# Optimization experiments

Measured on AMD Instinct MI355X. Metric: run time of the kernel, lower is better.

The kernel has to match this reference:

```python
import jax, jax.numpy as jnp
import numpy as np

B, S, D = 256, 512, 768
SEP_ID = 2
BOS_ID = 0
PAD_ID = 1


def setup_inputs() -> dict:
    key = jax.random.key(0)
    k_h, = jax.random.split(key, 1)
    hidden_states = jax.random.normal(k_h, (B, S, D), dtype=jnp.float32)

    rng = np.random.default_rng(0)
    ids = rng.integers(5, 64000, size=(B, S), dtype=np.int64)
    mask = np.zeros((B, S), dtype=np.int64)
    title_len = rng.integers(3, 60, size=B)
    lead_len = rng.integers(10, 300, size=B)
    for i in range(B):
        tl, ll = int(title_len[i]), int(lead_len[i])
        ids[i, 0] = BOS_ID
        ids[i, 1 + tl] = SEP_ID          # first </s>
        ids[i, 2 + tl] = SEP_ID          # second </s>
        lead_end = 3 + tl + ll           # position of third </s>
        lead_end = min(lead_end, S - 1)
        ids[i, 3 + tl:lead_end] = rng.integers(5, 64000, size=lead_end - (3 + tl))
        ids[i, lead_end] = SEP_ID        # third </s>
        ids[i, lead_end + 1:] = PAD_ID
        mask[i, :lead_end + 1] = 1
    return {
        "hidden_states": hidden_states,
        "input_ids": jnp.asarray(ids),
        "attention_mask": jnp.asarray(mask),
        "sep_token_id": SEP_ID,
    }


def reference(hidden_states, input_ids, attention_mask, sep_token_id):
    Bsz, Slen, _ = hidden_states.shape
    idx = jnp.arange(Slen)
    sep = input_ids == sep_token_id                     # [B,S] bool
    cnt = jnp.cumsum(sep.astype(jnp.int32), axis=1)     # running sep count

    def kth_sep_pos(k):
        # position of k-th sep token; Slen sentinel if absent
        return jnp.min(jnp.where(sep & (cnt == k), idx[None, :], Slen), axis=1)

    pos1, pos2, pos3 = kth_sep_pos(1), kth_sep_pos(2), kth_sep_pos(3)
    nsep = sep.sum(axis=1)
    attn_len = attention_mask.sum(axis=1).astype(jnp.int32)

    title_end = pos1                                   # title = tokens [1, title_end)
    lead_start = pos2 + 1
    lead_end = jnp.where(nsep >= 3, pos3, attn_len)    # lead = tokens [lead_start, lead_end)

    tmask = (idx[None, :] >= 1) & (idx[None, :] < title_end[:, None])
    lmask = (idx[None, :] >= lead_start[:, None]) & (idx[None, :] < lead_end[:, None])

    def masked_mean(m):
        mf = m.astype(hidden_states.dtype)
        n = mf.sum(axis=1)                             # [B]
        s = jnp.einsum('bs,bsd->bd', mf, hidden_states)
        return s / jnp.maximum(n, 1.0)[:, None], n

    tmean, tn = masked_mean(tmask)
    lmean, ln = masked_mean(lmask)

    cls = hidden_states[:, 0, :]
    valid = nsep >= 2
    title_pool = jnp.where((valid & (tn > 0))[:, None], tmean, cls)
    lead_pool = jnp.where((valid & (ln > 0))[:, None], lmean, cls)
    return title_pool, lead_pool
```

## Files before the change

### kernel.cpp

```cpp
#include <hip/hip_runtime.h>

#define BATCH 256
#define SEQ   512
#define DIM   768
#define D4    192
#define SPL   4
#define NTHR  (SPL * D4)

__global__ __launch_bounds__(NTHR) void seg_pool_fused(
    const float* __restrict__ hidden,
    const int*  __restrict__ ids,
    const int*  __restrict__ amask,
    const int*  __restrict__ sep_tok,
    float* __restrict__ out)
{
    const int b   = blockIdx.x;
    const int seg = blockIdx.y;
    const int t   = threadIdx.x;

    __shared__ int    s_info[2];
    __shared__ float4 s_red[SPL][D4];

    if (t < 64) {
        const int lane = t;
        const int sep  = sep_tok[0];

        int nsep = 0;
        int p0 = SEQ, p1 = SEQ, p2 = SEQ;
        int attn = 0;

        #pragma unroll
        for (int c = 0; c < SEQ / 64; ++c) {
            const int s  = c * 64 + lane;
            const int id = ids[b * SEQ + s];
            const int am = amask[b * SEQ + s];
            unsigned long long msep = __ballot(id == sep);
            unsigned long long mat  = __ballot(am != 0);
            attn += __popcll(mat);
            while (msep) {
                const int bit = __ffsll((long long)msep) - 1;
                const int pos = c * 64 + bit;
                if (nsep == 0)      p0 = pos;
                else if (nsep == 1) p1 = pos;
                else if (nsep == 2) p2 = pos;
                ++nsep;
                msep &= msep - 1;
            }
        }

        if (lane == 0) {
            const bool valid = (nsep >= 2);
            int start, n;
            if (seg == 0) {
                start = 1;
                n = p0 - 1;
                if (n < 0 || !valid) n = 0;
            } else {
                start = p1 + 1;
                const int lead_end = (nsep >= 3) ? p2 : attn;
                n = lead_end - start;
                if (n < 0 || !valid) n = 0;
            }
            s_info[0] = start;
            s_info[1] = n;
        }
    }
    __syncthreads();

    const int start = s_info[0];
    const int n     = s_info[1];

    const int split = t / D4;
    const int d4    = t % D4;

    const float4* __restrict__ h4 = (const float4*)hidden;
    const size_t base = (size_t)b * (SEQ * D4);

    const int chunk = (n + SPL - 1) / SPL;
    const int s0    = start + split * chunk;
    int s1          = s0 + chunk;
    const int send  = start + n;
    if (s1 > send) s1 = send;

    float4 acc = {0.f, 0.f, 0.f, 0.f};
    #pragma unroll 8
    for (int s = s0; s < s1; ++s) {
        const float4 v = h4[base + (size_t)s * D4 + d4];
        acc.x += v.x; acc.y += v.y; acc.z += v.z; acc.w += v.w;
    }
    s_red[split][d4] = acc;
    __syncthreads();

    if (t < D4) {
        float4 res;
        if (n > 0) {
            const float4 a0 = s_red[0][t];
            const float4 a1 = s_red[1][t];
            const float4 a2 = s_red[2][t];
            const float4 a3 = s_red[3][t];
            const float fn = (float)n;
            res.x = (a0.x + a1.x + a2.x + a3.x) / fn;
            res.y = (a0.y + a1.y + a2.y + a3.y) / fn;
            res.z = (a0.z + a1.z + a2.z + a3.z) / fn;
            res.w = (a0.w + a1.w + a2.w + a3.w) / fn;
        } else {
            res = h4[base + t];
        }
        float4* __restrict__ o4 = (float4*)out;
        o4[(size_t)seg * (BATCH * D4) + (size_t)b * D4 + t] = res;
    }
}

extern "C" void kernel_launch(void* const* d_in, const int* in_sizes, int n_in,
                              void* d_out, int out_size, void* d_ws, size_t ws_size,
                              hipStream_t stream) {
    const float* hidden  = (const float*)d_in[0];
    const int*   ids     = (const int*)d_in[1];
    const int*   amask   = (const int*)d_in[2];
    const int*   sep_tok = (const int*)d_in[3];
    float*       out     = (float*)d_out;

    seg_pool_fused<<<dim3(BATCH, 2), dim3(NTHR), 0, stream>>>(
        hidden, ids, amask, sep_tok, out);
}
```

Before: 31.39 us.

## Split feature dim across grid z and parallelize separator scan over all warps

```diff
diff --git a/kernel.cpp b/kernel.cpp
--- a/kernel.cpp
+++ b/kernel.cpp
@@ -4,8 +4,9 @@
 #define SEQ   512
 #define DIM   768
 #define D4    192
-#define SPL   4
-#define NTHR  (SPL * D4)
+#define NW    8
+#define NTHR  (NW * 64)
+#define ZCH   3
 
 __global__ __launch_bounds__(NTHR) void seg_pool_fused(
     const float* __restrict__ hidden,
@@ -14,70 +15,68 @@
     const int*  __restrict__ sep_tok,
     float* __restrict__ out)
 {
-    const int b   = blockIdx.x;
-    const int seg = blockIdx.y;
-    const int t   = threadIdx.x;
+    const int b    = blockIdx.x;
+    const int seg  = blockIdx.y;
+    const int z    = blockIdx.z;
+    const int t    = threadIdx.x;
+    const int w    = t >> 6;
+    const int lane = t & 63;
 
+    __shared__ unsigned long long s_msep[NW];
+    __shared__ int    s_att[NW];
     __shared__ int    s_info[2];
-    __shared__ float4 s_red[SPL][D4];
+    __shared__ float4 s_red[NW][64];
 
-    if (t < 64) {
-        const int lane = t;
-        const int sep  = sep_tok[0];
+    {
+        const int id = ids[b * SEQ + t];
+        const int am = amask[b * SEQ + t];
+        const unsigned long long m  = __ballot(id == sep_tok[0]);
+        const unsigned long long ma = __ballot(am != 0);
+        if (lane == 0) { s_msep[w] = m; s_att[w] = __popcll(ma); }
+    }
+    __syncthreads();
 
-        int nsep = 0;
-        int p0 = SEQ, p1 = SEQ, p2 = SEQ;
-        int attn = 0;
-
+    if (t == 0) {
+        int nsep = 0, p0 = SEQ, p1 = SEQ, p2 = SEQ, attn = 0;
         #pragma unroll
-        for (int c = 0; c < SEQ / 64; ++c) {
-            const int s  = c * 64 + lane;
-            const int id = ids[b * SEQ + s];
-            const int am = amask[b * SEQ + s];
-            unsigned long long msep = __ballot(id == sep);
-            unsigned long long mat  = __ballot(am != 0);
-            attn += __popcll(mat);
-            while (msep) {
-                const int bit = __ffsll((long long)msep) - 1;
+        for (int c = 0; c < NW; ++c) {
+            attn += s_att[c];
+            unsigned long long mm = s_msep[c];
+            while (mm) {
+                const int bit = __ffsll((long long)mm) - 1;
                 const int pos = c * 64 + bit;
                 if (nsep == 0)      p0 = pos;
                 else if (nsep == 1) p1 = pos;
                 else if (nsep == 2) p2 = pos;
                 ++nsep;
-                msep &= msep - 1;
+                mm &= mm - 1;
             }
         }
-
-        if (lane == 0) {
-            const bool valid = (nsep >= 2);
-            int start, n;
-            if (seg == 0) {
-                start = 1;
-                n = p0 - 1;
-                if (n < 0 || !valid) n = 0;
-            } else {
-                start = p1 + 1;
-                const int lead_end = (nsep >= 3) ? p2 : attn;
-                n = lead_end - start;
-                if (n < 0 || !valid) n = 0;
-            }
-            s_info[0] = start;
-            s_info[1] = n;
+        const bool valid = (nsep >= 2);
+        int start, n;
+        if (seg == 0) {
+            start = 1;
+            n = p0 - 1;
+        } else {
+            start = p1 + 1;
+            const int lead_end = (nsep >= 3) ? p2 : attn;
+            n = lead_end - start;
         }
+        if (n < 0 || !valid) n = 0;
+        s_info[0] = start;
+        s_info[1] = n;
     }
     __syncthreads();
 
     const int start = s_info[0];
     const int n     = s_info[1];
-
-    const int split = t / D4;
-    const int d4    = t % D4;
+    const int d4    = z * 64 + lane;
 
     const float4* __restrict__ h4 = (const float4*)hidden;
     const size_t base = (size_t)b * (SEQ * D4);
 
-    const int chunk = (n + SPL - 1) / SPL;
-    const int s0    = start + split * chunk;
+    const int chunk = (n + NW - 1) / NW;
+    const int s0    = start + w * chunk;
     int s1          = s0 + chunk;
     const int send  = start + n;
     if (s1 > send) s1 = send;
@@ -88,26 +87,26 @@
         const float4 v = h4[base + (size_t)s * D4 + d4];
         acc.x += v.x; acc.y += v.y; acc.z += v.z; acc.w += v.w;
     }
-    s_red[split][d4] = acc;
+    s_red[w][lane] = acc;
     __syncthreads();
 
-    if (t < D4) {
+    if (t < 64) {
         float4 res;
         if (n > 0) {
-            const float4 a0 = s_red[0][t];
-            const float4 a1 = s_red[1][t];
-            const float4 a2 = s_red[2][t];
-            const float4 a3 = s_red[3][t];
+            float4 a = {0.f, 0.f, 0.f, 0.f};
+            #pragma unroll
+            for (int c = 0; c < NW; ++c) {
+                const float4 v = s_red[c][t];
+                a.x += v.x; a.y += v.y; a.z += v.z; a.w += v.w;
+            }
             const float fn = (float)n;
-            res.x = (a0.x + a1.x + a2.x + a3.x) / fn;
-            res.y = (a0.y + a1.y + a2.y + a3.y) / fn;
-            res.z = (a0.z + a1.z + a2.z + a3.z) / fn;
-            res.w = (a0.w + a1.w + a2.w + a3.w) / fn;
+            res.x = a.x / fn; res.y = a.y / fn;
+            res.z = a.z / fn; res.w = a.w / fn;
         } else {
-            res = h4[base + t];
+            res = h4[base + d4];
         }
         float4* __restrict__ o4 = (float4*)out;
-        o4[(size_t)seg * (BATCH * D4) + (size_t)b * D4 + t] = res;
+        o4[(size_t)seg * (BATCH * D4) + (size_t)b * D4 + d4] = res;
     }
 }
 
@@ -120,6 +119,6 @@
     const int*   sep_tok = (const int*)d_in[3];
     float*       out     = (float*)d_out;
 
-    seg_pool_fused<<<dim3(BATCH, 2), dim3(NTHR), 0, stream>>>(
+    seg_pool_fused<<<dim3(BATCH, 2, ZCH), dim3(NTHR), 0, stream>>>(
         hidden, ids, amask, sep_tok, out);
 }
```

Result: faster. 30.72 us (-2.2%).
